# Kernel optimization log

Hardware: AMD Instinct MI355X
Metric: run time of the kernel (lower is better)

The kernel has to match this reference:

```python
import jax, jax.numpy as jnp
import numpy as np

B, N, FEAT, H, HID = 2, 2048, 128, 5, 3
D = H * HID  # 15
NEG_INF = -9e15


def _gat(x, adj, W, a, concat):
    # x: [B,N,Fin], W: [Fin,Fout], a: [2*Fout]
    Wh = jnp.einsum('bnf,fo->bno', x, W)
    Fo = W.shape[1]
    f1 = Wh @ a[:Fo]          # [B,N]
    f2 = Wh @ a[Fo:]          # [B,N]
    e = jax.nn.leaky_relu(f1[:, :, None] + f2[:, None, :], 0.2)  # [B,N,N]
    att = jax.nn.softmax(jnp.where(adj > 0, e, NEG_INF), axis=-1)
    h = jnp.einsum('bij,bjo->bio', att, Wh)
    return (jax.nn.elu(h) if concat else h), att


def _diff_pool(x, adj, s):
    # torch_geometric.dense_diff_pool
    s = jax.nn.softmax(s, axis=-1)                       # [B,N,K]
    out = jnp.einsum('bnk,bnf->bkf', s, x)               # [B,K,F]
    out_adj = jnp.einsum('bnk,bnm,bml->bkl', s, adj, s)  # [B,K,K]
    link = jnp.linalg.norm(adj - jnp.einsum('bnk,bmk->bnm', s, s)) / adj.size
    ent = jnp.mean(jnp.sum(-s * jnp.log(s + 1e-15), axis=-1))
    return out, out_adj, link, ent


def setup_inputs() -> dict:
    key = jax.random.key(0)
    ks = jax.random.split(key, 16)
    p = lambda k, shp: (jax.random.normal(k, shp, jnp.float32) * 0.1)
    d = {}
    d['x'] = jax.random.normal(ks[0], (B, N, FEAT), jnp.float32)
    d['adj'] = jax.random.bernoulli(ks[1], 0.05, (B, N, N)).astype(jnp.float32)
    d['W_heads'] = p(ks[2], (H, FEAT, HID))
    d['a_heads'] = p(ks[3], (H, 2 * HID))
    d['W_out'] = p(ks[4], (D, D)); d['a_out'] = p(ks[5], (2 * D,))
    d['W_p1'] = p(ks[6], (D, 32)); d['a_p1'] = p(ks[7], (64,))
    d['lin1_w'] = p(ks[8], (32, 32)); d['lin1_b'] = p(ks[9], (32,))
    d['W_p2'] = p(ks[10], (D, 4)); d['a_p2'] = p(ks[11], (8,))
    d['lin2_w'] = p(ks[12], (4, 4)); d['lin2_b'] = p(ks[13], (4,))
    d['lin_w'] = p(ks[14], (4 * D, 2)); d['lin_b'] = p(ks[15], (2,))
    return d


def reference(x, adj, W_heads, a_heads, W_out, a_out, W_p1, a_p1,
              lin1_w, lin1_b, W_p2, a_p2, lin2_w, lin2_b, lin_w, lin_b):
    # eval mode: dropout = identity
    hs, atts = jax.vmap(lambda W, a: _gat(x, adj, W, a, True))(W_heads, a_heads)
    # hs: [H,B,N,HID] -> concat heads -> [B,N,H*HID]
    h = jnp.moveaxis(hs, 0, 2).reshape(x.shape[0], x.shape[1], -1)
    h = jax.nn.elu(_gat(h, adj, W_out, a_out, False)[0])
    # pool 1: N -> 32 clusters
    s1 = _gat(h, adj, W_p1, a_p1, True)[0] @ lin1_w + lin1_b
    h, adj2, link1, ent1 = _diff_pool(h, adj, s1)
    # pool 2: 32 -> 4 clusters
    s2 = _gat(h, adj2, W_p2, a_p2, True)[0] @ lin2_w + lin2_b
    h, adj3, link2, ent2 = _diff_pool(h, adj2, s2)
    ypred = h.reshape(h.shape[0], -1) @ lin_w + lin_b  # [B, class_num]
    loss = link1 + link2
    return ypred, loss, atts
```

## Files before the change

### kernel.cpp

```cpp
#include <hip/hip_runtime.h>
#include <hip/hip_bf16.h>

#define NN 2048
#define BB 2
#define RB 4096
#define CAP 192

__device__ __forceinline__ float lrelu(float v) { return v > 0.f ? v : 0.2f * v; }
__device__ __forceinline__ float eluf(float v) { return v > 0.f ? v : __expf(v) - 1.f; }

__device__ __forceinline__ float wredsum(float v) {
    for (int o = 32; o; o >>= 1) v += __shfl_down(v, o, 64);
    return v;
}
__device__ __forceinline__ float bsum(float v) {
    for (int m = 32; m; m >>= 1) v += __shfl_xor(v, m, 64);
    return v;
}
__device__ __forceinline__ float bmax(float v) {
    for (int m = 32; m; m >>= 1) v = fmaxf(v, __shfl_xor(v, m, 64));
    return v;
}

__global__ void k_zero(float* S) { if (threadIdx.x < 2) S[threadIdx.x] = 0.f; }

__global__ __launch_bounds__(256) void k_prep1(const float* __restrict__ x,
                                               const float* __restrict__ W,
                                               const float* __restrict__ a,
                                               float* __restrict__ Wh1,
                                               float* __restrict__ f1o,
                                               float* __restrict__ f2o) {
    const int tid = threadIdx.x, w = tid >> 6, lane = tid & 63;
    const int r = blockIdx.x * 4 + w;
    const float xa = x[(size_t)r * 128 + lane];
    const float xb = x[(size_t)r * 128 + 64 + lane];
#pragma unroll
    for (int h = 0; h < 5; ++h) {
        float f1v = 0.f, f2v = 0.f;
#pragma unroll
        for (int f = 0; f < 3; ++f) {
            const float w0 = W[h * 384 + lane * 3 + f];
            const float w1 = W[h * 384 + (lane + 64) * 3 + f];
            const float d = bsum(xa * w0 + xb * w1);
            if (lane == 0) Wh1[((size_t)h * RB + r) * 3 + f] = d;
            f1v += d * a[h * 6 + f];
            f2v += d * a[h * 6 + 3 + f];
        }
        if (lane == 0) { f1o[h * RB + r] = f1v; f2o[h * RB + r] = f2v; }
    }
}

__global__ __launch_bounds__(320) void k_gat1(const float* __restrict__ adj,
                                              const float* __restrict__ Wh,
                                              const float* __restrict__ f1,
                                              const float* __restrict__ f2,
                                              const float* __restrict__ W_out,
                                              const float* __restrict__ a_out,
                                              float* __restrict__ Wh2,
                                              float* __restrict__ f1_2,
                                              float* __restrict__ f2_2,
                                              float* __restrict__ att_out,
                                              int* __restrict__ nnzcnt,
                                              unsigned short* __restrict__ nnzidx,
                                              float* __restrict__ S) {
    __shared__ float dense[5][2052];
    __shared__ unsigned short nidx[CAP];
    __shared__ float h1row[15];
    __shared__ int ncnt;
    const int tid = threadIdx.x, h = tid >> 6, lane = tid & 63;
    const int r = blockIdx.x;
    const int b = r >> 11, i = r & (NN - 1);
    const float* arow = adj + ((size_t)b * NN + i) * NN;

    if (tid == 0) ncnt = 0;
    __syncthreads();
    for (int j = tid; j < NN; j += 320) {
        if (arow[j] > 0.f) {
            const int pos = atomicAdd(&ncnt, 1);
            if (pos < CAP) nidx[pos] = (unsigned short)j;
        }
    }
    __syncthreads();
    const int cnt = min(ncnt, CAP);
    if (tid == 0) { nnzcnt[r] = cnt; atomicAdd(S, (float)ncnt); }
    for (int p = tid; p < cnt; p += 320) nnzidx[(size_t)r * CAP + p] = nidx[p];

    float4* dz = (float4*)dense[h];
#pragma unroll
    for (int v = lane; v < 513; v += 64) dz[v] = make_float4(0.f, 0.f, 0.f, 0.f);

    const float f1i = f1[h * RB + r];
    const float* f2h = f2 + h * RB + b * NN;
    const float* WhB = Wh + ((size_t)h * RB + b * NN) * 3;
    float lsum = 0.f, h0 = 0.f, h1v = 0.f, h2v = 0.f;
    for (int q = lane; q < cnt; q += 64) {
        const int j = nidx[q];
        const float p = __expf(lrelu(f1i + f2h[j]));
        dense[h][j + 1] = p;
        lsum += p;
        const float* wv = WhB + (size_t)j * 3;
        h0 += p * wv[0]; h1v += p * wv[1]; h2v += p * wv[2];
    }
    const float inv = 1.f / bsum(lsum);
    h0 = bsum(h0); h1v = bsum(h1v); h2v = bsum(h2v);
    if (lane == 0) {
        h1row[h * 3 + 0] = eluf(h0 * inv);
        h1row[h * 3 + 1] = eluf(h1v * inv);
        h1row[h * 3 + 2] = eluf(h2v * inv);
    }
    float* ao = att_out + (((size_t)h * BB + b) * NN + i) * NN;
    if (lane < 3) ao[lane] = dense[h][1 + lane] * inv;
    float4* ao4 = (float4*)(ao + 3);
    const float4* dh4 = (const float4*)dense[h];
    for (int v = lane; v < 511; v += 64) {
        const float4 d = dh4[1 + v];
        ao4[v] = make_float4(d.x * inv, d.y * inv, d.z * inv, d.w * inv);
    }
    if (lane == 63) ao[2047] = dense[h][2048] * inv;

    __syncthreads();
    if (h == 0) {
        float whv = 0.f;
        if (lane < 15) {
#pragma unroll
            for (int f = 0; f < 15; f++) whv += h1row[f] * W_out[f * 15 + lane];
            Wh2[(size_t)r * 15 + lane] = whv;
        }
        float s1p = (lane < 15) ? whv * a_out[lane] : 0.f;
        float s2p = (lane < 15) ? whv * a_out[15 + lane] : 0.f;
        s1p = wredsum(s1p); s2p = wredsum(s2p);
        if (lane == 0) { f1_2[r] = s1p; f2_2[r] = s2p; }
    }
}

__global__ __launch_bounds__(256) void k_gat2(const int* __restrict__ nnzcnt,
                                              const unsigned short* __restrict__ nnzidx,
                                              const float* __restrict__ Wh2,
                                              const float* __restrict__ f1_2,
                                              const float* __restrict__ f2_2,
                                              const float* __restrict__ W_p1,
                                              const float* __restrict__ a_p1,
                                              float* __restrict__ h2,
                                              float* __restrict__ Wh3,
                                              float* __restrict__ f1_3,
                                              float* __restrict__ f2_3) {
    __shared__ unsigned short sidx[4][CAP];
    __shared__ float sp[4][CAP];
    __shared__ float h2l[4][15];
    const int tid = threadIdx.x, w = tid >> 6, lane = tid & 63;
    const int r = blockIdx.x * 4 + w;
    const int b = r >> 11;
    const int cnt = nnzcnt[r];
    for (int q = lane; q < cnt; q += 64) sidx[w][q] = nnzidx[(size_t)r * CAP + q];
    __syncthreads();

    const float f1i = f1_2[r];
    float ee[3];
    float lm = -3.0e38f;
#pragma unroll
    for (int t3 = 0; t3 < 3; ++t3) {
        const int q = lane + 64 * t3;
        if (q < cnt) {
            const int j = sidx[w][q];
            const float v = lrelu(f1i + f2_2[b * NN + j]);
            ee[t3] = v;
            lm = fmaxf(lm, v);
        } else ee[t3] = -3.0e38f;
    }
    const float m = bmax(lm);
    float lsum = 0.f;
#pragma unroll
    for (int t3 = 0; t3 < 3; ++t3) {
        const int q = lane + 64 * t3;
        if (q < cnt) {
            const float p = __expf(ee[t3] - m);
            sp[w][q] = p;
            lsum += p;
        }
    }
    const float inv = 1.f / bsum(lsum);
    __syncthreads();

    const int g4 = lane / 15, f = lane - g4 * 15;
    float acc = 0.f;
    if (lane < 60) {
        for (int q = g4; q < cnt; q += 4)
            acc += sp[w][q] * Wh2[(size_t)(b * NN + sidx[w][q]) * 15 + f];
    }
    acc += __shfl_down(acc, 15, 64);
    acc += __shfl_down(acc, 30, 64);
    if (lane < 15) {
        const float v = eluf(acc * inv);
        h2[(size_t)r * 15 + f] = v;
        h2l[w][f] = v;
    }
    __syncthreads();

    float wh3 = 0.f;
    if (lane < 32) {
#pragma unroll
        for (int ff = 0; ff < 15; ++ff) wh3 += h2l[w][ff] * W_p1[ff * 32 + lane];
        Wh3[(size_t)r * 32 + lane] = wh3;
    }
    float s1p = (lane < 32) ? wh3 * a_p1[lane] : 0.f;
    float s2p = (lane < 32) ? wh3 * a_p1[32 + lane] : 0.f;
    s1p = bsum(s1p); s2p = bsum(s2p);
    if (lane == 0) { f1_3[r] = s1p; f2_3[r] = s2p; }
}

__global__ __launch_bounds__(256) void k_gat3(const int* __restrict__ nnzcnt,
                                              const unsigned short* __restrict__ nnzidx,
                                              const float* __restrict__ Wh3,
                                              const float* __restrict__ f1_3,
                                              const float* __restrict__ f2_3,
                                              const float* __restrict__ lw,
                                              const float* __restrict__ lb,
                                              float* __restrict__ s_out) {
    __shared__ unsigned short sidx[4][CAP];
    __shared__ float sp[4][CAP];
    __shared__ float h3l[4][32];
    const int tid = threadIdx.x, w = tid >> 6, lane = tid & 63;
    const int r = blockIdx.x * 4 + w;
    const int b = r >> 11;
    const int cnt = nnzcnt[r];
    for (int q = lane; q < cnt; q += 64) sidx[w][q] = nnzidx[(size_t)r * CAP + q];
    __syncthreads();

    const float f1i = f1_3[r];
    float ee[3];
    float lm = -3.0e38f;
#pragma unroll
    for (int t3 = 0; t3 < 3; ++t3) {
        const int q = lane + 64 * t3;
        if (q < cnt) {
            const int j = sidx[w][q];
            const float v = lrelu(f1i + f2_3[b * NN + j]);
            ee[t3] = v;
            lm = fmaxf(lm, v);
        } else ee[t3] = -3.0e38f;
    }
    const float m = bmax(lm);
    float lsum = 0.f;
#pragma unroll
    for (int t3 = 0; t3 < 3; ++t3) {
        const int q = lane + 64 * t3;
        if (q < cnt) {
            const float p = __expf(ee[t3] - m);
            sp[w][q] = p;
            lsum += p;
        }
    }
    const float inv = 1.f / bsum(lsum);
    __syncthreads();

    const int g2 = lane >> 5, f = lane & 31;
    float acc = 0.f;
    for (int q = g2; q < cnt; q += 2)
        acc += sp[w][q] * Wh3[(size_t)(b * NN + sidx[w][q]) * 32 + f];
    acc += __shfl_xor(acc, 32, 64);
    if (lane < 32) h3l[w][f] = eluf(acc * inv);
    __syncthreads();

    float z = -3.0e38f;
    if (lane < 32) {
        z = lb[lane];
#pragma unroll
        for (int ff = 0; ff < 32; ++ff) z += h3l[w][ff] * lw[ff * 32 + lane];
    }
    const float zm = bmax(z);
    const float p2 = (lane < 32) ? __expf(z - zm) : 0.f;
    const float zinv = 1.f / bsum(p2);
    if (lane < 32) s_out[(size_t)r * 32 + lane] = p2 * zinv;
}

__global__ __launch_bounds__(256) void k_tsp(const int* __restrict__ nnzcnt,
                                             const unsigned short* __restrict__ nnzidx,
                                             const float* __restrict__ smat,
                                             float* __restrict__ t) {
    __shared__ unsigned short sidx[4][CAP];
    const int tid = threadIdx.x, w = tid >> 6, lane = tid & 63;
    const int r = blockIdx.x * 4 + w;
    const int b = r >> 11;
    const int cnt = nnzcnt[r];
    for (int q = lane; q < cnt; q += 64) sidx[w][q] = nnzidx[(size_t)r * CAP + q];
    __syncthreads();
    const int g2 = lane >> 5, f = lane & 31;
    float acc = 0.f;
    for (int q = g2; q < cnt; q += 2)
        acc += smat[(size_t)(b * NN + sidx[w][q]) * 32 + f];
    acc += __shfl_xor(acc, 32, 64);
    if (lane < 32) t[(size_t)r * 32 + f] = acc;
}

__global__ __launch_bounds__(256) void k_gram2(const float* __restrict__ s,
                                               const float* __restrict__ t,
                                               float* __restrict__ adj2,
                                               float* __restrict__ S) {
    const int bk = blockIdx.x;
    const int b = bk >> 5, k = bk & 31;
    const int tid = threadIdx.x, lane = tid & 63, wid = tid >> 6;
    __shared__ float redG[128], redT[128];
    __shared__ float gsq[32], tval[32];
    float aG[32], aT[32];
#pragma unroll
    for (int l = 0; l < 32; l++) { aG[l] = 0.f; aT[l] = 0.f; }
    const float* sb = s + (size_t)b * NN * 32;
    const float* tb = t + (size_t)b * NN * 32;
    for (int n = tid; n < NN; n += 256) {
        const float sv = sb[(size_t)n * 32 + k];
        const float* sj = sb + (size_t)n * 32;
        const float* tj = tb + (size_t)n * 32;
#pragma unroll
        for (int l = 0; l < 32; l++) { aG[l] += sv * sj[l]; aT[l] += sv * tj[l]; }
    }
#pragma unroll
    for (int l = 0; l < 32; l++) {
        const float vG = wredsum(aG[l]);
        const float vT = wredsum(aT[l]);
        if (lane == 0) { redG[wid * 32 + l] = vG; redT[wid * 32 + l] = vT; }
    }
    __syncthreads();
    if (tid < 32) {
        const float G = redG[tid] + redG[32 + tid] + redG[64 + tid] + redG[96 + tid];
        const float T = redT[tid] + redT[32 + tid] + redT[64 + tid] + redT[96 + tid];
        adj2[((size_t)b * 32 + k) * 32 + tid] = T;
        gsq[tid] = G * G;
        tval[tid] = T;
    }
    __syncthreads();
    if (tid == 0) {
        float ss = 0.f;
#pragma unroll
        for (int l = 0; l < 32; l++) ss += gsq[l];
        atomicAdd(S, ss - 2.f * tval[k]);
    }
}

__global__ __launch_bounds__(256) void k_hp1(const float* __restrict__ s,
                                             const float* __restrict__ h2,
                                             float* __restrict__ hp1) {
    const int bk = blockIdx.x;
    const int b = bk >> 5, k = bk & 31;
    const int tid = threadIdx.x, lane = tid & 63, wid = tid >> 6;
    __shared__ float red[64];
    float acc[15];
#pragma unroll
    for (int f = 0; f < 15; f++) acc[f] = 0.f;
    const float* sb = s + (size_t)b * NN * 32;
    const float* hb = h2 + (size_t)b * NN * 15;
    for (int j = tid; j < NN; j += 256) {
        const float sv = sb[(size_t)j * 32 + k];
        const float* hj = hb + (size_t)j * 15;
#pragma unroll
        for (int f = 0; f < 15; f++) acc[f] += sv * hj[f];
    }
#pragma unroll
    for (int f = 0; f < 15; f++) {
        const float v = wredsum(acc[f]);
        if (lane == 0) red[wid * 15 + f] = v;
    }
    __syncthreads();
    if (tid < 15) hp1[((size_t)b * 32 + k) * 15 + tid] = red[tid] + red[15 + tid] + red[30 + tid] + red[45 + tid];
}

__global__ __launch_bounds__(64) void k_pool2(const float* __restrict__ hp1,
                                              const float* __restrict__ adj2,
                                              const float* __restrict__ Wp2, const float* __restrict__ a2,
                                              const float* __restrict__ l2w, const float* __restrict__ l2b,
                                              const float* __restrict__ lw, const float* __restrict__ lb,
                                              float* __restrict__ S2, float* __restrict__ out) {
    __shared__ float hp[480], a2l[1024], wh[128], f1l[32], f2l[32], s2l[128], hp2[60];
    const int b = blockIdx.x, tid = threadIdx.x;
    for (int idx = tid; idx < 480; idx += 64) hp[idx] = hp1[b * 480 + idx];
    for (int idx = tid; idx < 1024; idx += 64) a2l[idx] = adj2[b * 1024 + idx];
    __syncthreads();
    for (int idx = tid; idx < 128; idx += 64) {
        const int n = idx >> 2, c = idx & 3;
        float acc = 0.f;
#pragma unroll
        for (int f = 0; f < 15; f++) acc += hp[n * 15 + f] * Wp2[f * 4 + c];
        wh[idx] = acc;
    }
    __syncthreads();
    if (tid < 32) {
        float s1 = 0.f, s2 = 0.f;
#pragma unroll
        for (int c = 0; c < 4; c++) {
            s1 += wh[tid * 4 + c] * a2[c];
            s2 += wh[tid * 4 + c] * a2[4 + c];
        }
        f1l[tid] = s1;
        f2l[tid] = s2;
    }
    __syncthreads();
    if (tid < 32) {
        const int n = tid;
        float e[32];
        float m = -3.0e38f;
#pragma unroll
        for (int j = 0; j < 32; j++) {
            const float v = lrelu(f1l[n] + f2l[j]);
            e[j] = a2l[n * 32 + j] > 0.f ? v : -9.0e15f;
            m = fmaxf(m, e[j]);
        }
        float sum = 0.f;
#pragma unroll
        for (int j = 0; j < 32; j++) { e[j] = __expf(e[j] - m); sum += e[j]; }
        const float inv = 1.f / sum;
        float h4[4];
#pragma unroll
        for (int c = 0; c < 4; c++) {
            float acc = 0.f;
#pragma unroll
            for (int j = 0; j < 32; j++) acc += e[j] * wh[j * 4 + c];
            h4[c] = eluf(acc * inv);
        }
        float z[4];
        float zm = -3.0e38f;
#pragma unroll
        for (int c = 0; c < 4; c++) {
            float acc = l2b[c];
#pragma unroll
            for (int c2 = 0; c2 < 4; c2++) acc += h4[c2] * l2w[c2 * 4 + c];
            z[c] = acc;
            zm = fmaxf(zm, acc);
        }
        float zs = 0.f;
#pragma unroll
        for (int c = 0; c < 4; c++) { z[c] = __expf(z[c] - zm); zs += z[c]; }
        const float zi = 1.f / zs;
#pragma unroll
        for (int c = 0; c < 4; c++) s2l[n * 4 + c] = z[c] * zi;
    }
    __syncthreads();
    if (tid < 60) {
        const int c = tid / 15, f = tid % 15;
        float acc = 0.f;
#pragma unroll
        for (int n = 0; n < 32; n++) acc += s2l[n * 4 + c] * hp[n * 15 + f];
        hp2[tid] = acc;
    }
    float lacc = 0.f;
    for (int idx = tid; idx < 1024; idx += 64) {
        const int n = idx >> 5, mm = idx & 31;
        float d = 0.f;
#pragma unroll
        for (int c = 0; c < 4; c++) d += s2l[n * 4 + c] * s2l[mm * 4 + c];
        const float df = a2l[idx] - d;
        lacc += df * df;
    }
    lacc = wredsum(lacc);
    if (tid == 0) atomicAdd(S2, lacc);
    __syncthreads();
    if (tid < 2) {
        float acc = lb[tid];
#pragma unroll
        for (int k2 = 0; k2 < 60; k2++) acc += hp2[k2] * lw[k2 * 2 + tid];
        out[b * 2 + tid] = acc;
    }
}

__global__ void k_final(const float* __restrict__ S, float* __restrict__ out) {
    const float loss = sqrtf(S[0]) / 8388608.f + sqrtf(S[1]) / 2048.f;
    out[4] = loss;
}

extern "C" void kernel_launch(void* const* d_in, const int* in_sizes, int n_in,
                              void* d_out, int out_size, void* d_ws, size_t ws_size,
                              hipStream_t stream) {
    const float* x      = (const float*)d_in[0];
    const float* adj    = (const float*)d_in[1];
    const float* W_h    = (const float*)d_in[2];
    const float* a_h    = (const float*)d_in[3];
    const float* W_out  = (const float*)d_in[4];
    const float* a_out  = (const float*)d_in[5];
    const float* W_p1   = (const float*)d_in[6];
    const float* a_p1   = (const float*)d_in[7];
    const float* lin1_w = (const float*)d_in[8];
    const float* lin1_b = (const float*)d_in[9];
    const float* W_p2   = (const float*)d_in[10];
    const float* a_p2   = (const float*)d_in[11];
    const float* lin2_w = (const float*)d_in[12];
    const float* lin2_b = (const float*)d_in[13];
    const float* lin_w  = (const float*)d_in[14];
    const float* lin_b  = (const float*)d_in[15];
    float* outp = (float*)d_out;

    float* W = (float*)d_ws;
    float* Wh1  = W;
    float* f1_1 = Wh1 + 61440;
    float* f2_1 = f1_1 + 20480;
    float* Wh2  = f2_1 + 20480;
    float* f1_2 = Wh2 + 61440;
    float* f2_2 = f1_2 + 4096;
    float* h2   = f2_2 + 4096;
    float* Wh3  = h2 + 61440;
    float* f1_3 = Wh3 + 131072;
    float* f2_3 = f1_3 + 4096;
    float* s    = f2_3 + 4096;
    float* t    = s + 131072;
    float* hp1  = t + 131072;
    float* adj2 = hp1 + 960;
    float* S    = adj2 + 2048;
    int* nnzcnt = (int*)(S + 2);
    unsigned short* nnzidx = (unsigned short*)(nnzcnt + RB);

    k_zero<<<1, 64, 0, stream>>>(S);
    k_prep1<<<RB / 4, 256, 0, stream>>>(x, W_h, a_h, Wh1, f1_1, f2_1);
    k_gat1<<<RB, 320, 0, stream>>>(adj, Wh1, f1_1, f2_1, W_out, a_out,
                                   Wh2, f1_2, f2_2, outp + 5, nnzcnt, nnzidx, S);
    k_gat2<<<RB / 4, 256, 0, stream>>>(nnzcnt, nnzidx, Wh2, f1_2, f2_2,
                                       W_p1, a_p1, h2, Wh3, f1_3, f2_3);
    k_gat3<<<RB / 4, 256, 0, stream>>>(nnzcnt, nnzidx, Wh3, f1_3, f2_3,
                                       lin1_w, lin1_b, s);
    k_tsp<<<RB / 4, 256, 0, stream>>>(nnzcnt, nnzidx, s, t);
    k_gram2<<<64, 256, 0, stream>>>(s, t, adj2, S);
    k_hp1<<<64, 256, 0, stream>>>(s, h2, hp1);
    k_pool2<<<BB, 64, 0, stream>>>(hp1, adj2, W_p2, a_p2, lin2_w, lin2_b, lin_w, lin_b, S + 1, outp);
    k_final<<<1, 1, 0, stream>>>(S, outp);
}
```

Measured before the change: 177.7 us.

## Split dense attention write into separate scatter kernel and fuse pooling stats

The first GAT kernel no longer builds a dense 5x2048 shared-memory row and writes the attention matrix. It now stores only the per-row softmax inverse. A new scatter kernel, one block per head-row, zeroes the output row and writes the nonzero attention values, recomputing exp from f1/f2. The gram and pooled-feature reductions are merged into one kernel so s is read once. This frees large LDS for occupancy in the gather kernel, at the cost of an extra launch and writing the output rows in two passes (zero fill, then scatter).

```diff
diff --git a/kernel.cpp b/kernel.cpp
--- a/kernel.cpp
+++ b/kernel.cpp
@@ -50,7 +50,7 @@
     }
 }
 
-__global__ __launch_bounds__(320) void k_gat1(const float* __restrict__ adj,
+__global__ __launch_bounds__(320) void k_gata(const float* __restrict__ adj,
                                               const float* __restrict__ Wh,
                                               const float* __restrict__ f1,
                                               const float* __restrict__ f2,
@@ -59,11 +59,10 @@
                                               float* __restrict__ Wh2,
                                               float* __restrict__ f1_2,
                                               float* __restrict__ f2_2,
-                                              float* __restrict__ att_out,
+                                              float* __restrict__ sinv,
                                               int* __restrict__ nnzcnt,
                                               unsigned short* __restrict__ nnzidx,
                                               float* __restrict__ S) {
-    __shared__ float dense[5][2052];
     __shared__ unsigned short nidx[CAP];
     __shared__ float h1row[15];
     __shared__ int ncnt;
@@ -85,10 +84,6 @@
     if (tid == 0) { nnzcnt[r] = cnt; atomicAdd(S, (float)ncnt); }
     for (int p = tid; p < cnt; p += 320) nnzidx[(size_t)r * CAP + p] = nidx[p];
 
-    float4* dz = (float4*)dense[h];
-#pragma unroll
-    for (int v = lane; v < 513; v += 64) dz[v] = make_float4(0.f, 0.f, 0.f, 0.f);
-
     const float f1i = f1[h * RB + r];
     const float* f2h = f2 + h * RB + b * NN;
     const float* WhB = Wh + ((size_t)h * RB + b * NN) * 3;
@@ -96,7 +91,6 @@
     for (int q = lane; q < cnt; q += 64) {
         const int j = nidx[q];
         const float p = __expf(lrelu(f1i + f2h[j]));
-        dense[h][j + 1] = p;
         lsum += p;
         const float* wv = WhB + (size_t)j * 3;
         h0 += p * wv[0]; h1v += p * wv[1]; h2v += p * wv[2];
@@ -104,20 +98,11 @@
     const float inv = 1.f / bsum(lsum);
     h0 = bsum(h0); h1v = bsum(h1v); h2v = bsum(h2v);
     if (lane == 0) {
+        sinv[h * RB + r] = inv;
         h1row[h * 3 + 0] = eluf(h0 * inv);
         h1row[h * 3 + 1] = eluf(h1v * inv);
         h1row[h * 3 + 2] = eluf(h2v * inv);
     }
-    float* ao = att_out + (((size_t)h * BB + b) * NN + i) * NN;
-    if (lane < 3) ao[lane] = dense[h][1 + lane] * inv;
-    float4* ao4 = (float4*)(ao + 3);
-    const float4* dh4 = (const float4*)dense[h];
-    for (int v = lane; v < 511; v += 64) {
-        const float4 d = dh4[1 + v];
-        ao4[v] = make_float4(d.x * inv, d.y * inv, d.z * inv, d.w * inv);
-    }
-    if (lane == 63) ao[2047] = dense[h][2048] * inv;
-
     __syncthreads();
     if (h == 0) {
         float whv = 0.f;
@@ -130,6 +115,33 @@
         float s2p = (lane < 15) ? whv * a_out[15 + lane] : 0.f;
         s1p = wredsum(s1p); s2p = wredsum(s2p);
         if (lane == 0) { f1_2[r] = s1p; f2_2[r] = s2p; }
+    }
+}
+
+__global__ __launch_bounds__(256) void k_scatter(const float* __restrict__ f1,
+                                                 const float* __restrict__ f2,
+                                                 const float* __restrict__ sinv,
+                                                 const int* __restrict__ nnzcnt,
+                                                 const unsigned short* __restrict__ nnzidx,
+                                                 float* __restrict__ att_out) {
+    const int idx = blockIdx.x;
+    const int h = idx >> 12;
+    const int r = idx & (RB - 1);
+    const int b = r >> 11, i = r & (NN - 1);
+    const int tid = threadIdx.x;
+    float* ao = att_out + (((size_t)h * BB + b) * NN + i) * NN;
+    if (tid < 3) ao[tid] = 0.f;
+    if (tid == 3) ao[2047] = 0.f;
+    float4* ao4 = (float4*)(ao + 3);
+    for (int v = tid; v < 511; v += 256) ao4[v] = make_float4(0.f, 0.f, 0.f, 0.f);
+    __syncthreads();
+    const int cnt = nnzcnt[r];
+    const float f1i = f1[h * RB + r];
+    const float* f2h = f2 + h * RB + b * NN;
+    const float inv = sinv[h * RB + r];
+    for (int q = tid; q < cnt; q += 256) {
+        const int j = nnzidx[(size_t)r * CAP + q];
+        ao[j] = __expf(lrelu(f1i + f2h[j])) * inv;
     }
 }
 
@@ -292,32 +304,45 @@
     if (lane < 32) t[(size_t)r * 32 + f] = acc;
 }
 
-__global__ __launch_bounds__(256) void k_gram2(const float* __restrict__ s,
-                                               const float* __restrict__ t,
-                                               float* __restrict__ adj2,
-                                               float* __restrict__ S) {
+__global__ __launch_bounds__(256) void k_pstats(const float* __restrict__ s,
+                                                const float* __restrict__ t,
+                                                const float* __restrict__ h2,
+                                                float* __restrict__ adj2,
+                                                float* __restrict__ hp1,
+                                                float* __restrict__ S) {
     const int bk = blockIdx.x;
     const int b = bk >> 5, k = bk & 31;
     const int tid = threadIdx.x, lane = tid & 63, wid = tid >> 6;
-    __shared__ float redG[128], redT[128];
+    __shared__ float redG[128], redT[128], redH[60];
     __shared__ float gsq[32], tval[32];
-    float aG[32], aT[32];
+    float aG[32], aT[32], aH[15];
 #pragma unroll
     for (int l = 0; l < 32; l++) { aG[l] = 0.f; aT[l] = 0.f; }
+#pragma unroll
+    for (int f = 0; f < 15; f++) aH[f] = 0.f;
     const float* sb = s + (size_t)b * NN * 32;
     const float* tb = t + (size_t)b * NN * 32;
+    const float* hb = h2 + (size_t)b * NN * 15;
     for (int n = tid; n < NN; n += 256) {
         const float sv = sb[(size_t)n * 32 + k];
         const float* sj = sb + (size_t)n * 32;
         const float* tj = tb + (size_t)n * 32;
+        const float* hj = hb + (size_t)n * 15;
 #pragma unroll
         for (int l = 0; l < 32; l++) { aG[l] += sv * sj[l]; aT[l] += sv * tj[l]; }
+#pragma unroll
+        for (int f = 0; f < 15; f++) aH[f] += sv * hj[f];
     }
 #pragma unroll
     for (int l = 0; l < 32; l++) {
         const float vG = wredsum(aG[l]);
         const float vT = wredsum(aT[l]);
         if (lane == 0) { redG[wid * 32 + l] = vG; redT[wid * 32 + l] = vT; }
+    }
+#pragma unroll
+    for (int f = 0; f < 15; f++) {
+        const float vH = wredsum(aH[f]);
+        if (lane == 0) redH[wid * 15 + f] = vH;
     }
     __syncthreads();
     if (tid < 32) {
@@ -327,6 +352,7 @@
         gsq[tid] = G * G;
         tval[tid] = T;
     }
+    if (tid < 15) hp1[((size_t)b * 32 + k) * 15 + tid] = redH[tid] + redH[15 + tid] + redH[30 + tid] + redH[45 + tid];
     __syncthreads();
     if (tid == 0) {
         float ss = 0.f;
@@ -334,33 +360,6 @@
         for (int l = 0; l < 32; l++) ss += gsq[l];
         atomicAdd(S, ss - 2.f * tval[k]);
     }
-}
-
-__global__ __launch_bounds__(256) void k_hp1(const float* __restrict__ s,
-                                             const float* __restrict__ h2,
-                                             float* __restrict__ hp1) {
-    const int bk = blockIdx.x;
-    const int b = bk >> 5, k = bk & 31;
-    const int tid = threadIdx.x, lane = tid & 63, wid = tid >> 6;
-    __shared__ float red[64];
-    float acc[15];
-#pragma unroll
-    for (int f = 0; f < 15; f++) acc[f] = 0.f;
-    const float* sb = s + (size_t)b * NN * 32;
-    const float* hb = h2 + (size_t)b * NN * 15;
-    for (int j = tid; j < NN; j += 256) {
-        const float sv = sb[(size_t)j * 32 + k];
-        const float* hj = hb + (size_t)j * 15;
-#pragma unroll
-        for (int f = 0; f < 15; f++) acc[f] += sv * hj[f];
-    }
-#pragma unroll
-    for (int f = 0; f < 15; f++) {
-        const float v = wredsum(acc[f]);
-        if (lane == 0) red[wid * 15 + f] = v;
-    }
-    __syncthreads();
-    if (tid < 15) hp1[((size_t)b * 32 + k) * 15 + tid] = red[tid] + red[15 + tid] + red[30 + tid] + red[45 + tid];
 }
 
 __global__ __launch_bounds__(64) void k_pool2(const float* __restrict__ hp1,
@@ -502,20 +501,21 @@
     float* hp1  = t + 131072;
     float* adj2 = hp1 + 960;
     float* S    = adj2 + 2048;
-    int* nnzcnt = (int*)(S + 2);
+    float* sinv = S + 2;
+    int* nnzcnt = (int*)(sinv + 20480);
     unsigned short* nnzidx = (unsigned short*)(nnzcnt + RB);
 
     k_zero<<<1, 64, 0, stream>>>(S);
     k_prep1<<<RB / 4, 256, 0, stream>>>(x, W_h, a_h, Wh1, f1_1, f2_1);
-    k_gat1<<<RB, 320, 0, stream>>>(adj, Wh1, f1_1, f2_1, W_out, a_out,
-                                   Wh2, f1_2, f2_2, outp + 5, nnzcnt, nnzidx, S);
+    k_gata<<<RB, 320, 0, stream>>>(adj, Wh1, f1_1, f2_1, W_out, a_out,
+                                   Wh2, f1_2, f2_2, sinv, nnzcnt, nnzidx, S);
+    k_scatter<<<5 * RB, 256, 0, stream>>>(f1_1, f2_1, sinv, nnzcnt, nnzidx, outp + 5);
     k_gat2<<<RB / 4, 256, 0, stream>>>(nnzcnt, nnzidx, Wh2, f1_2, f2_2,
                                        W_p1, a_p1, h2, Wh3, f1_3, f2_3);
     k_gat3<<<RB / 4, 256, 0, stream>>>(nnzcnt, nnzidx, Wh3, f1_3, f2_3,
                                        lin1_w, lin1_b, s);
     k_tsp<<<RB / 4, 256, 0, stream>>>(nnzcnt, nnzidx, s, t);
-    k_gram2<<<64, 256, 0, stream>>>(s, t, adj2, S);
-    k_hp1<<<64, 256, 0, stream>>>(s, h2, hp1);
+    k_pstats<<<64, 256, 0, stream>>>(s, t, h2, adj2, hp1, S);
     k_pool2<<<BB, 64, 0, stream>>>(hp1, adj2, W_p2, a_p2, lin2_w, lin2_b, lin_w, lin_b, S + 1, outp);
     k_final<<<1, 1, 0, stream>>>(S, outp);
 }
```

New measurement: 209.7 us. 18.0% more time.
